# Kernel optimization log

Measured on AMD Instinct MI355X. Metric: run time of the kernel, lower is better.

## Reference

```python
import jax, jax.numpy as jnp
import numpy as np

N_NODES = 100000
N_EDGES = 1600000
D_IN = 128
D_OUT = 128


def setup_inputs() -> dict:
    key = jax.random.key(0)
    k_x, k_s, k_r, k_w = jax.random.split(key, 4)
    x = jax.random.normal(k_x, (N_NODES, D_IN), dtype=jnp.float32)
    senders = jax.random.randint(k_s, (N_EDGES,), 0, N_NODES, dtype=jnp.int32)
    receivers = jax.random.randint(k_r, (N_EDGES,), 0, N_NODES, dtype=jnp.int32)
    # xavier_uniform for (D_IN, D_OUT)
    limit = float(np.sqrt(6.0 / (D_IN + D_OUT)))
    weight = jax.random.uniform(k_w, (D_IN, D_OUT), dtype=jnp.float32,
                                minval=-limit, maxval=limit)
    bias = jnp.zeros((D_OUT,), dtype=jnp.float32)
    return {"x": x, "senders": senders, "receivers": receivers,
            "n_node": N_NODES, "weight": weight, "bias": bias}


def reference(x, senders, receivers, n_node, weight, bias):
    # Linear node update: [N, D_in] @ [D_in, D_out] + bias
    h = jnp.dot(x, weight) + bias
    total_num_nodes = x.shape[0]

    # Degree counts via segment_sum of ones (symmetric normalization)
    ones = jnp.ones_like(senders)
    sender_degree = jax.ops.segment_sum(ones, senders, num_segments=total_num_nodes)
    receiver_degree = jax.ops.segment_sum(ones, receivers, num_segments=total_num_nodes)

    # Pre-scale by 1/sqrt(deg_out), scatter-sum along edges, post-scale by 1/sqrt(deg_in)
    h = h * jax.lax.rsqrt(jnp.maximum(sender_degree, 1.0))[:, None]
    agg = jax.ops.segment_sum(h[senders], receivers, num_segments=total_num_nodes)
    out = agg * jax.lax.rsqrt(jnp.maximum(receiver_degree, 1.0))[:, None]
    return out
```

## Files before the change

kernel.cpp:

```cpp
#include <hip/hip_runtime.h>
#include <hip/hip_bf16.h>
#include <stdint.h>

#define N_NODES 100000
#define N_EDGES 1600000
#define TILE 8192
#define NB 196
#define BIN_BLOCKS ((N_EDGES + TILE - 1) / TILE)

static const size_t OFF_H      = 0;
static const size_t OFF_SSCALE = 25600000;
static const size_t OFF_ROWP   = 26000000;
static const size_t OFF_RHIST  = 26400016;
static const size_t OFF_SHIST  = 26401040;
static const size_t OFF_RBASE  = 26402064;
static const size_t OFF_SBASE  = 26403088;
static const size_t OFF_RCUR   = 26404112;
static const size_t OFF_SCUR   = 26405136;
static const size_t OFF_WFRAG  = 26406160;
static const size_t OFF_EBUF   = 26438928;
static const size_t OFF_SBUF   = 32838928;

using short8 = __attribute__((ext_vector_type(8))) short;
using f32x4  = __attribute__((ext_vector_type(4))) float;

static __device__ __forceinline__ short f2bf(float f) {
    uint32_t u = __float_as_uint(f);
    uint32_t r = (u + 0x7fffu + ((u >> 16) & 1u)) >> 16;
    return (short)r;
}

__global__ __launch_bounds__(256) void prep_w_kernel(const float* __restrict__ W,
                                                     short8* __restrict__ wfrag) {
    int slot = blockIdx.x * 256 + threadIdx.x;
    int f = slot >> 6, lane = slot & 63;
    int quad = lane >> 4, mcol = lane & 15;
    int s = f >> 3, c = f & 7;
    int krow = s * 32 + quad * 8;
    int ncol = c * 16 + mcol;
    short8 wf;
    #pragma unroll
    for (int j = 0; j < 8; j++)
        wf[j] = f2bf(W[(krow + j) * 128 + ncol]);
    wfrag[slot] = wf;
}

__global__ __launch_bounds__(256) void hist196_kernel(const int* __restrict__ snd,
                                                      const int* __restrict__ rcv,
                                                      int* __restrict__ rhist,
                                                      int* __restrict__ shist) {
    __shared__ int hr[256], hs[256];
    int t = threadIdx.x;
    hr[t] = 0; hs[t] = 0;
    __syncthreads();
    int base = blockIdx.x * TILE;
    #pragma unroll
    for (int j = 0; j < 32; j++) {
        int idx = base + j * 256 + t;
        if (idx < N_EDGES) {
            atomicAdd(&hr[rcv[idx] >> 9], 1);
            atomicAdd(&hs[snd[idx] >> 9], 1);
        }
    }
    __syncthreads();
    if (t < NB) {
        if (hr[t]) atomicAdd(&rhist[t], hr[t]);
        if (hs[t]) atomicAdd(&shist[t], hs[t]);
    }
}

__global__ __launch_bounds__(256) void scanb_kernel(const int* __restrict__ rhist,
                                                    const int* __restrict__ shist,
                                                    int* __restrict__ rbase,
                                                    int* __restrict__ sbase,
                                                    int* __restrict__ rcur,
                                                    int* __restrict__ scur,
                                                    int* __restrict__ row_ptr) {
    __shared__ int s[256];
    int t = threadIdx.x;

    int v = (t < NB) ? rhist[t] : 0;
    s[t] = v;
    __syncthreads();
    #pragma unroll
    for (int off = 1; off < 256; off <<= 1) {
        int tv = (t >= off) ? s[t - off] : 0;
        __syncthreads();
        s[t] += tv;
        __syncthreads();
    }
    if (t < NB) { int e = s[t] - v; rbase[t] = e; rcur[t] = e; }
    __syncthreads();

    v = (t < NB) ? shist[t] : 0;
    s[t] = v;
    __syncthreads();
    #pragma unroll
    for (int off = 1; off < 256; off <<= 1) {
        int tv = (t >= off) ? s[t - off] : 0;
        __syncthreads();
        s[t] += tv;
        __syncthreads();
    }
    if (t < NB) { int e = s[t] - v; sbase[t] = e; scur[t] = e; }
    if (t == 0) row_ptr[N_NODES] = N_EDGES;
}

__global__ __launch_bounds__(256) void binr_kernel(const int* __restrict__ snd,
                                                   const int* __restrict__ rcv,
                                                   int* __restrict__ rcur,
                                                   int* __restrict__ scur,
                                                   uint32_t* __restrict__ ebuf,
                                                   uint16_t* __restrict__ sbuf) {
    __shared__ int hist[256];
    __shared__ int coff[256];
    __shared__ int ccur[256];
    __shared__ int gbase[256];
    __shared__ uint32_t stage[TILE];

    const int t = threadIdx.x;
    const int base = blockIdx.x * TILE;

    uint32_t ss[32], rs[32];
    #pragma unroll
    for (int j = 0; j < 32; j++) {
        int idx = base + j * 256 + t;
        bool ok = idx < N_EDGES;
        ss[j] = ok ? (uint32_t)snd[idx] : 0u;
        rs[j] = ok ? (uint32_t)rcv[idx] : 0xffffffffu;
    }

    hist[t] = 0;
    __syncthreads();
    #pragma unroll
    for (int j = 0; j < 32; j++)
        if (rs[j] != 0xffffffffu) atomicAdd(&hist[rs[j] >> 9], 1);
    __syncthreads();

    int v = hist[t];
    ccur[t] = v;
    __syncthreads();
    #pragma unroll
    for (int off = 1; off < 256; off <<= 1) {
        int tv = (t >= off) ? ccur[t - off] : 0;
        __syncthreads();
        ccur[t] += tv;
        __syncthreads();
    }
    int excl = ccur[t] - v;
    coff[t] = excl;
    int gb = 0;
    if (v > 0) gb = atomicAdd(&rcur[t], v);
    gbase[t] = gb - excl;
    __syncthreads();
    ccur[t] = excl;
    __syncthreads();

    #pragma unroll
    for (int j = 0; j < 32; j++) {
        uint32_t r = rs[j];
        if (r != 0xffffffffu) {
            int pos = atomicAdd(&ccur[r >> 9], 1);
            stage[pos] = (ss[j] << 9) | (r & 511u);
        }
    }
    __syncthreads();

    int total = coff[255] + hist[255];
    for (int i = t; i < total; i += 256) {
        uint32_t pv = stage[i];
        int lo = 0;
        #pragma unroll
        for (int step = 128; step; step >>= 1)
            if (lo + step < 256 && coff[lo + step] <= i) lo += step;
        ebuf[gbase[lo] + i] = pv;
    }
    __syncthreads();

    hist[t] = 0;
    __syncthreads();
    #pragma unroll
    for (int j = 0; j < 32; j++)
        if (rs[j] != 0xffffffffu) atomicAdd(&hist[ss[j] >> 9], 1);
    __syncthreads();

    v = hist[t];
    ccur[t] = v;
    __syncthreads();
    #pragma unroll
    for (int off = 1; off < 256; off <<= 1) {
        int tv = (t >= off) ? ccur[t - off] : 0;
        __syncthreads();
        ccur[t] += tv;
        __syncthreads();
    }
    excl = ccur[t] - v;
    coff[t] = excl;
    gb = 0;
    if (v > 0) gb = atomicAdd(&scur[t], v);
    gbase[t] = gb - excl;
    __syncthreads();
    ccur[t] = excl;
    __syncthreads();

    uint16_t* stage16 = (uint16_t*)stage;
    #pragma unroll
    for (int j = 0; j < 32; j++) {
        if (rs[j] != 0xffffffffu) {
            int pos = atomicAdd(&ccur[ss[j] >> 9], 1);
            stage16[pos] = (uint16_t)(ss[j] & 511u);
        }
    }
    __syncthreads();

    total = coff[255] + hist[255];
    for (int i = t; i < total; i += 256) {
        uint16_t pv = stage16[i];
        int lo = 0;
        #pragma unroll
        for (int step = 128; step; step >>= 1)
            if (lo + step < 256 && coff[lo + step] <= i) lo += step;
        sbuf[gbase[lo] + i] = pv;
    }
}

__global__ __launch_bounds__(256) void bucket_kernel(const int* __restrict__ rbase,
                                                     const int* __restrict__ rhist,
                                                     const int* __restrict__ sbase,
                                                     const int* __restrict__ shist,
                                                     uint32_t* __restrict__ ebuf,
                                                     const uint16_t* __restrict__ sbuf,
                                                     int* __restrict__ row_ptr,
                                                     float* __restrict__ sscale) {
    __shared__ int hist_l[512];
    __shared__ int excl_l[512];
    __shared__ int cur_l[512];
    __shared__ int ps[256];
    __shared__ uint32_t inb[9216];
    __shared__ uint32_t perm[9216];

    const int b = blockIdx.x;
    const int t = threadIdx.x;
    const int nbase = b << 9;
    const int base = rbase[b];
    const int size = rhist[b];

    hist_l[t] = 0; hist_l[t + 256] = 0;
    __syncthreads();

    for (int i = t; i < size; i += 256) {
        uint32_t v = ebuf[base + i];
        inb[i] = v;
        atomicAdd(&hist_l[v & 511u], 1);
    }
    __syncthreads();

    int h0 = hist_l[2 * t], h1 = hist_l[2 * t + 1];
    int p = h0 + h1;
    ps[t] = p;
    __syncthreads();
    #pragma unroll
    for (int off = 1; off < 256; off <<= 1) {
        int tv = (t >= off) ? ps[t - off] : 0;
        __syncthreads();
        ps[t] += tv;
        __syncthreads();
    }
    int pe = ps[t] - p;
    excl_l[2 * t] = pe;
    excl_l[2 * t + 1] = pe + h0;
    cur_l[2 * t] = pe;
    cur_l[2 * t + 1] = pe + h0;
    __syncthreads();

    for (int i = t; i < 512; i += 256) {
        int n = nbase + i;
        if (n < N_NODES) row_ptr[n] = base + excl_l[i];
    }

    for (int i = t; i < size; i += 256) {
        uint32_t v = inb[i];
        int pos = atomicAdd(&cur_l[v & 511u], 1);
        perm[pos] = v >> 9;
    }
    __syncthreads();
    for (int i = t; i < size; i += 256)
        ebuf[base + i] = perm[i];

    __syncthreads();
    hist_l[t] = 0; hist_l[t + 256] = 0;
    __syncthreads();
    const int sb = sbase[b];
    const int ssz = shist[b];
    for (int i = t; i < ssz; i += 256)
        atomicAdd(&hist_l[(int)sbuf[sb + i]], 1);
    __syncthreads();
    for (int i = t; i < 512; i += 256) {
        int n = nbase + i;
        if (n < N_NODES) sscale[n] = rsqrtf(fmaxf((float)hist_l[i], 1.f));
    }
}

__global__ __launch_bounds__(256, 3) void gemm_mfma_kernel(const float* __restrict__ x,
                                                           const short8* __restrict__ wfrag,
                                                           const float* __restrict__ bias,
                                                           const float* __restrict__ sscale,
                                                           short* __restrict__ h) {
    const int t = threadIdx.x;
    const int lane = t & 63;
    const int wv = t >> 6;
    const int quad = lane >> 4;
    const int mcol = lane & 15;

    const int node0 = blockIdx.x * 128 + wv * 32;
    short8 afrag[2][4];
    #pragma unroll
    for (int mf = 0; mf < 2; mf++) {
        int node = node0 + mf * 16 + mcol;
        bool ok = node < N_NODES;
        const float* xr = x + (size_t)(ok ? node : 0) * 128;
        #pragma unroll
        for (int s = 0; s < 4; s++) {
            int k0 = s * 32 + quad * 8;
            f32x4 v0 = ok ? *(const f32x4*)(xr + k0)     : f32x4{0.f,0.f,0.f,0.f};
            f32x4 v1 = ok ? *(const f32x4*)(xr + k0 + 4) : f32x4{0.f,0.f,0.f,0.f};
            short8 af;
            #pragma unroll
            for (int j = 0; j < 4; j++) {
                af[j]     = f2bf(v0[j]);
                af[4 + j] = f2bf(v1[j]);
            }
            afrag[mf][s] = af;
        }
    }

    f32x4 acc[2][8];
    #pragma unroll
    for (int mf = 0; mf < 2; mf++)
        #pragma unroll
        for (int c = 0; c < 8; c++)
            acc[mf][c] = f32x4{0.f, 0.f, 0.f, 0.f};

    #pragma unroll
    for (int s = 0; s < 4; s++) {
        #pragma unroll
        for (int c = 0; c < 8; c++) {
            short8 bfrag = wfrag[(s * 8 + c) * 64 + lane];
            acc[0][c] = __builtin_amdgcn_mfma_f32_16x16x32_bf16(afrag[0][s], bfrag, acc[0][c], 0, 0, 0);
            acc[1][c] = __builtin_amdgcn_mfma_f32_16x16x32_bf16(afrag[1][s], bfrag, acc[1][c], 0, 0, 0);
        }
    }

    float rsv[2][4];
    #pragma unroll
    for (int mf = 0; mf < 2; mf++)
        #pragma unroll
        for (int r = 0; r < 4; r++) {
            int nd = node0 + mf * 16 + quad * 4 + r;
            rsv[mf][r] = (nd < N_NODES) ? sscale[nd] : 1.f;
        }

    #pragma unroll
    for (int mf = 0; mf < 2; mf++)
        #pragma unroll
        for (int c = 0; c < 8; c++) {
            float bval = bias[c * 16 + mcol];
            #pragma unroll
            for (int r = 0; r < 4; r++) {
                int nd = node0 + mf * 16 + quad * 4 + r;
                if (nd < N_NODES)
                    h[(size_t)nd * 128 + c * 16 + mcol] =
                        f2bf((acc[mf][c][r] + bval) * rsv[mf][r]);
            }
        }
}

__global__ __launch_bounds__(256) void gather_kernel(const uint32_t* __restrict__ h2,
                                                     const int* __restrict__ row_ptr,
                                                     const uint32_t* __restrict__ esrc,
                                                     float4* __restrict__ out4) {
    int wv = threadIdx.x >> 6;
    int lane = threadIdx.x & 63;
    int half = lane >> 5;
    int ln = lane & 31;
    int node = blockIdx.x * 8 + wv * 2 + half;

    int b = row_ptr[node];
    int e = row_ptr[node + 1];
    float a0 = 0.f, a1 = 0.f, a2 = 0.f, a3 = 0.f;
    int i = b;
    for (; i + 4 <= e; i += 4) {
        uint32_t s0 = esrc[i + 0], s1 = esrc[i + 1], s2 = esrc[i + 2], s3 = esrc[i + 3];
        uint2 v0 = *(const uint2*)&h2[(size_t)s0 * 64 + ln * 2];
        uint2 v1 = *(const uint2*)&h2[(size_t)s1 * 64 + ln * 2];
        uint2 v2 = *(const uint2*)&h2[(size_t)s2 * 64 + ln * 2];
        uint2 v3 = *(const uint2*)&h2[(size_t)s3 * 64 + ln * 2];
        a0 += __uint_as_float(v0.x << 16) + __uint_as_float(v1.x << 16)
            + __uint_as_float(v2.x << 16) + __uint_as_float(v3.x << 16);
        a1 += __uint_as_float(v0.x & 0xffff0000u) + __uint_as_float(v1.x & 0xffff0000u)
            + __uint_as_float(v2.x & 0xffff0000u) + __uint_as_float(v3.x & 0xffff0000u);
        a2 += __uint_as_float(v0.y << 16) + __uint_as_float(v1.y << 16)
            + __uint_as_float(v2.y << 16) + __uint_as_float(v3.y << 16);
        a3 += __uint_as_float(v0.y & 0xffff0000u) + __uint_as_float(v1.y & 0xffff0000u)
            + __uint_as_float(v2.y & 0xffff0000u) + __uint_as_float(v3.y & 0xffff0000u);
    }
    for (; i < e; i++) {
        uint32_t s = esrc[i];
        uint2 v = *(const uint2*)&h2[(size_t)s * 64 + ln * 2];
        a0 += __uint_as_float(v.x << 16);
        a1 += __uint_as_float(v.x & 0xffff0000u);
        a2 += __uint_as_float(v.y << 16);
        a3 += __uint_as_float(v.y & 0xffff0000u);
    }
    float rs = rsqrtf(fmaxf((float)(e - b), 1.f));
    out4[(size_t)node * 32 + ln] = make_float4(a0 * rs, a1 * rs, a2 * rs, a3 * rs);
}

extern "C" void kernel_launch(void* const* d_in, const int* in_sizes, int n_in,
                              void* d_out, int out_size, void* d_ws, size_t ws_size,
                              hipStream_t stream) {
    const float* x    = (const float*)d_in[0];
    const int*   snd  = (const int*)d_in[1];
    const int*   rcv  = (const int*)d_in[2];
    const float* W    = (const float*)d_in[4];
    const float* bias = (const float*)d_in[5];

    char* ws = (char*)d_ws;
    short*    h      = (short*)(ws + OFF_H);
    float*    sscale = (float*)(ws + OFF_SSCALE);
    int*      rowp   = (int*)(ws + OFF_ROWP);
    int*      rhist  = (int*)(ws + OFF_RHIST);
    int*      shist  = (int*)(ws + OFF_SHIST);
    int*      rbase  = (int*)(ws + OFF_RBASE);
    int*      sbase  = (int*)(ws + OFF_SBASE);
    int*      rcur   = (int*)(ws + OFF_RCUR);
    int*      scur   = (int*)(ws + OFF_SCUR);
    short8*   wfrag  = (short8*)(ws + OFF_WFRAG);
    uint32_t* ebuf   = (uint32_t*)(ws + OFF_EBUF);
    uint16_t* sbuf   = (uint16_t*)(ws + OFF_SBUF);

    hipMemsetAsync(ws + OFF_RHIST, 0, 2048, stream);

    prep_w_kernel  <<<8, 256, 0, stream>>>(W, wfrag);
    hist196_kernel <<<BIN_BLOCKS, 256, 0, stream>>>(snd, rcv, rhist, shist);
    scanb_kernel   <<<1, 256, 0, stream>>>(rhist, shist, rbase, sbase, rcur, scur, rowp);
    binr_kernel    <<<BIN_BLOCKS, 256, 0, stream>>>(snd, rcv, rcur, scur, ebuf, sbuf);
    bucket_kernel  <<<NB, 256, 0, stream>>>(rbase, rhist, sbase, shist, ebuf, sbuf, rowp, sscale);
    gemm_mfma_kernel<<<(N_NODES + 127) / 128, 256, 0, stream>>>(x, wfrag, bias, sscale, h);
    gather_kernel  <<<N_NODES / 8, 256, 0, stream>>>((const uint32_t*)h, rowp, ebuf, (float4*)d_out);
}
```

Before: 272.3 us.

## Sort per-node edge lists and widen gather to 16-byte loads with 16 lanes per node

After the bucket permutation, each thread insertion-sorts the source indices within its receiver segments so that gathers from the same node visit sources in ascending order, which should give better cache and DRAM locality. The gather kernel now uses 16 lanes per node, each loading a uint4 (8 bf16 values), so a wave handles 4 nodes instead of 2 with fewer, wider load instructions. The per-thread serial insertion sort adds work and shared-memory traffic to the bucket kernel, and the wider loads mean fewer lanes are issuing memory requests for each node.

```diff
diff --git a/kernel.cpp b/kernel.cpp
--- a/kernel.cpp
+++ b/kernel.cpp
@@ -29,6 +29,8 @@
     uint32_t r = (u + 0x7fffu + ((u >> 16) & 1u)) >> 16;
     return (short)r;
 }
+static __device__ __forceinline__ float bflo(uint32_t u) { return __uint_as_float(u << 16); }
+static __device__ __forceinline__ float bfhi(uint32_t u) { return __uint_as_float(u & 0xffff0000u); }
 
 __global__ __launch_bounds__(256) void prep_w_kernel(const float* __restrict__ W,
                                                      short8* __restrict__ wfrag) {
@@ -284,6 +286,19 @@
         perm[pos] = v >> 9;
     }
     __syncthreads();
+
+    for (int seg = t; seg < 512; seg += 256) {
+        int s0 = excl_l[seg];
+        int s1 = cur_l[seg];
+        for (int i2 = s0 + 1; i2 < s1; i2++) {
+            uint32_t key = perm[i2];
+            int j = i2 - 1;
+            while (j >= s0 && perm[j] > key) { perm[j + 1] = perm[j]; j--; }
+            perm[j + 1] = key;
+        }
+    }
+    __syncthreads();
+
     for (int i = t; i < size; i += 256)
         ebuf[base + i] = perm[i];
 
@@ -375,45 +390,47 @@
         }
 }
 
-__global__ __launch_bounds__(256) void gather_kernel(const uint32_t* __restrict__ h2,
+__global__ __launch_bounds__(256) void gather_kernel(const uint4* __restrict__ hrow,
                                                      const int* __restrict__ row_ptr,
                                                      const uint32_t* __restrict__ esrc,
                                                      float4* __restrict__ out4) {
     int wv = threadIdx.x >> 6;
     int lane = threadIdx.x & 63;
-    int half = lane >> 5;
-    int ln = lane & 31;
-    int node = blockIdx.x * 8 + wv * 2 + half;
+    int q = lane >> 4;
+    int ln = lane & 15;
+    int node = blockIdx.x * 16 + wv * 4 + q;
 
     int b = row_ptr[node];
     int e = row_ptr[node + 1];
-    float a0 = 0.f, a1 = 0.f, a2 = 0.f, a3 = 0.f;
+    float a0=0.f,a1=0.f,a2=0.f,a3=0.f,a4=0.f,a5=0.f,a6=0.f,a7=0.f;
     int i = b;
     for (; i + 4 <= e; i += 4) {
         uint32_t s0 = esrc[i + 0], s1 = esrc[i + 1], s2 = esrc[i + 2], s3 = esrc[i + 3];
-        uint2 v0 = *(const uint2*)&h2[(size_t)s0 * 64 + ln * 2];
-        uint2 v1 = *(const uint2*)&h2[(size_t)s1 * 64 + ln * 2];
-        uint2 v2 = *(const uint2*)&h2[(size_t)s2 * 64 + ln * 2];
-        uint2 v3 = *(const uint2*)&h2[(size_t)s3 * 64 + ln * 2];
-        a0 += __uint_as_float(v0.x << 16) + __uint_as_float(v1.x << 16)
-            + __uint_as_float(v2.x << 16) + __uint_as_float(v3.x << 16);
-        a1 += __uint_as_float(v0.x & 0xffff0000u) + __uint_as_float(v1.x & 0xffff0000u)
-            + __uint_as_float(v2.x & 0xffff0000u) + __uint_as_float(v3.x & 0xffff0000u);
-        a2 += __uint_as_float(v0.y << 16) + __uint_as_float(v1.y << 16)
-            + __uint_as_float(v2.y << 16) + __uint_as_float(v3.y << 16);
-        a3 += __uint_as_float(v0.y & 0xffff0000u) + __uint_as_float(v1.y & 0xffff0000u)
-            + __uint_as_float(v2.y & 0xffff0000u) + __uint_as_float(v3.y & 0xffff0000u);
+        uint4 v0 = hrow[(size_t)s0 * 16 + ln];
+        uint4 v1 = hrow[(size_t)s1 * 16 + ln];
+        uint4 v2 = hrow[(size_t)s2 * 16 + ln];
+        uint4 v3 = hrow[(size_t)s3 * 16 + ln];
+        a0 += bflo(v0.x) + bflo(v1.x) + bflo(v2.x) + bflo(v3.x);
+        a1 += bfhi(v0.x) + bfhi(v1.x) + bfhi(v2.x) + bfhi(v3.x);
+        a2 += bflo(v0.y) + bflo(v1.y) + bflo(v2.y) + bflo(v3.y);
+        a3 += bfhi(v0.y) + bfhi(v1.y) + bfhi(v2.y) + bfhi(v3.y);
+        a4 += bflo(v0.z) + bflo(v1.z) + bflo(v2.z) + bflo(v3.z);
+        a5 += bfhi(v0.z) + bfhi(v1.z) + bfhi(v2.z) + bfhi(v3.z);
+        a6 += bflo(v0.w) + bflo(v1.w) + bflo(v2.w) + bflo(v3.w);
+        a7 += bfhi(v0.w) + bfhi(v1.w) + bfhi(v2.w) + bfhi(v3.w);
     }
     for (; i < e; i++) {
         uint32_t s = esrc[i];
-        uint2 v = *(const uint2*)&h2[(size_t)s * 64 + ln * 2];
-        a0 += __uint_as_float(v.x << 16);
-        a1 += __uint_as_float(v.x & 0xffff0000u);
-        a2 += __uint_as_float(v.y << 16);
-        a3 += __uint_as_float(v.y & 0xffff0000u);
+        uint4 v = hrow[(size_t)s * 16 + ln];
+        a0 += bflo(v.x); a1 += bfhi(v.x);
+        a2 += bflo(v.y); a3 += bfhi(v.y);
+        a4 += bflo(v.z); a5 += bfhi(v.z);
+        a6 += bflo(v.w); a7 += bfhi(v.w);
     }
     float rs = rsqrtf(fmaxf((float)(e - b), 1.f));
-    out4[(size_t)node * 32 + ln] = make_float4(a0 * rs, a1 * rs, a2 * rs, a3 * rs);
+    size_t o = (size_t)node * 32 + ln * 2;
+    out4[o]     = make_float4(a0 * rs, a1 * rs, a2 * rs, a3 * rs);
+    out4[o + 1] = make_float4(a4 * rs, a5 * rs, a6 * rs, a7 * rs);
 }
 
 extern "C" void kernel_launch(void* const* d_in, const int* in_sizes, int n_in,
@@ -447,5 +464,5 @@
     binr_kernel    <<<BIN_BLOCKS, 256, 0, stream>>>(snd, rcv, rcur, scur, ebuf, sbuf);
     bucket_kernel  <<<NB, 256, 0, stream>>>(rbase, rhist, sbase, shist, ebuf, sbuf, rowp, sscale);
     gemm_mfma_kernel<<<(N_NODES + 127) / 128, 256, 0, stream>>>(x, wfrag, bias, sscale, h);
-    gather_kernel  <<<N_NODES / 8, 256, 0, stream>>>((const uint32_t*)h, rowp, ebuf, (float4*)d_out);
-}
+    gather_kernel  <<<N_NODES / 16, 256, 0, stream>>>((const uint4*)h, rowp, ebuf, (float4*)d_out);
+}
```

New measurement: 341.1 us. 25.3% more time.
